# Optimization experiments

Hardware: AMD Instinct MI355X
Metric: run time of the kernel (lower is better)

The kernel has to match this reference:

```python
import jax, jax.numpy as jnp
import numpy as np

NEG_INF = float(-2 ** 31)
B, S, D_IN, D_H, H = 4, 2048, 512, 512, 8


def setup_inputs() -> dict:
    key = jax.random.key(0)
    ks = jax.random.split(key, 11)
    sc_in = 1.0 / np.sqrt(D_IN)
    sc_pr = 1.0 / np.sqrt(D_H * H)
    x = jax.random.normal(ks[0], (B, S, D_IN), dtype=jnp.float32)
    mask = jax.random.randint(ks[1], (B, 1, S), 0, 2, dtype=jnp.int32)
    Wq = jax.random.uniform(ks[2], (H, D_IN, D_H), jnp.float32, -sc_in, sc_in)
    bq = jax.random.uniform(ks[3], (H, D_H), jnp.float32, -sc_in, sc_in)
    Wk = jax.random.uniform(ks[4], (H, D_IN, D_H), jnp.float32, -sc_in, sc_in)
    bk = jax.random.uniform(ks[5], (H, D_H), jnp.float32, -sc_in, sc_in)
    Wv = jax.random.uniform(ks[6], (H, D_IN, D_H), jnp.float32, -sc_in, sc_in)
    bv = jax.random.uniform(ks[7], (H, D_H), jnp.float32, -sc_in, sc_in)
    Wp = jax.random.uniform(ks[8], (H * D_H, D_H), jnp.float32, -sc_pr, sc_pr)
    bp = jax.random.uniform(ks[9], (D_H,), jnp.float32, -sc_pr, sc_pr)
    return {"x": x, "mask": mask, "Wq": Wq, "bq": bq, "Wk": Wk, "bk": bk,
            "Wv": Wv, "bv": bv, "Wp": Wp, "bp": bp}


def reference(x, mask, Wq, bq, Wk, bk, Wv, bv, Wp, bp):
    # per-head Q/K/V projections, batched over the head axis h
    q = jnp.einsum('bsd,hde->bhse', x, Wq) + bq[None, :, None, :]
    k = jnp.einsum('bsd,hde->bhse', x, Wk) + bk[None, :, None, :]
    v = jnp.einsum('bsd,hde->bhse', x, Wv) + bv[None, :, None, :]
    scores = jnp.einsum('bhse,bhte->bhst', q, k) / jnp.sqrt(jnp.float32(D_H))
    scores = jnp.where(mask[:, None, :, :] == 0, NEG_INF, scores)
    probs = jax.nn.softmax(scores, axis=-1)
    out = jnp.einsum('bhst,bhte->bhse', probs, v)  # [B,H,S,D_H]
    cat = out.transpose(0, 2, 1, 3).reshape(B, S, H * D_H)
    return cat @ Wp + bp
```

## Files before the change

### kernel.cpp

```cpp
#include <hip/hip_runtime.h>
#include <hip/hip_bf16.h>
#include <cstdint>
#include <cstddef>

typedef unsigned short ushort_t;
typedef __bf16 bf16x8 __attribute__((ext_vector_type(8)));
typedef float floatx4 __attribute__((ext_vector_type(4)));

#define S_LEN 2048
#define DIN   512
#define DH    512
#define NHEAD 8
#define NBAT  4
#define NBH   32
#define HP    4096

#define MiB (1024ull * 1024ull)
#define WQT_OFF   (0ull)
#define WKT_OFF   (4ull  * MiB)
#define WVT_OFF   (8ull  * MiB)
#define WPT_OFF   (12ull * MiB)
#define XBF_OFF   (16ull * MiB)
#define Q_OFF     (24ull * MiB)
#define K_OFF     (88ull * MiB)
#define VT_OFF    (152ull * MiB)
#define O_OFF     (216ull * MiB)
#define LSUM_OFF  (280ull * MiB)
#define P_OFF     (281ull * MiB)
#define WS_BYTES  (409ull * MiB)

__device__ __align__(256) unsigned char g_ws[WS_BYTES];

__device__ __forceinline__ ushort_t f2bf(float f) {
  union { float f; uint32_t u; } v; v.f = f;
  uint32_t r = v.u + 0x7fffu + ((v.u >> 16) & 1u);
  return (ushort_t)(r >> 16);
}

typedef __attribute__((address_space(3))) uint32_t lds_uint;
typedef __attribute__((address_space(1))) const uint32_t glb_uint;

__device__ __forceinline__ void async16(void* lds, const void* g) {
  __builtin_amdgcn_global_load_lds((glb_uint*)g, (lds_uint*)lds, 16, 0, 0);
}

#define BBAR() do { \
    __builtin_amdgcn_sched_barrier(0); \
    __builtin_amdgcn_s_barrier(); \
    __builtin_amdgcn_sched_barrier(0); \
  } while (0)

#define SG_R(n) __builtin_amdgcn_sched_group_barrier(0x100, (n), 0)
#define SG_M(n) __builtin_amdgcn_sched_group_barrier(0x8,   (n), 0)
#define SG_V(n) __builtin_amdgcn_sched_group_barrier(0x10,  (n), 0)


#define STG_A(dbuf, hh, kt) do { \
    const ushort_t* _g = gA + (size_t)(kt) * 64 + (size_t)(hh) * a128; \
    char* _s = sAh + (dbuf) * 32768 + (hh) * 16384; \
    async16(_s, _g); \
    async16(_s + 8192, _g + a64); \
  } while (0)

#define STG_B(dbuf, hh, kt) do { \
    const ushort_t* _g = gB + (size_t)(kt) * 64 + (size_t)(hh) * b128; \
    char* _s = sBh + (dbuf) * 32768 + (hh) * 16384; \
    async16(_s, _g); \
    async16(_s + 8192, _g + b64); \
  } while (0)

#define LDAF(fi) do { \
    const char* _b = (const char*)As + cur * 32768 + ((fi) >> 2) * 16384 \
                     + (((fi) & 3) << 11) + aoff0; \
    af[fi][0] = *(const bf16x8*)(_b + swz0); \
    af[fi][1] = *(const bf16x8*)(_b + swz1); \
  } while (0)

#define LDBF(fj) do { \
    const char* _b = (const char*)Bs + cur * 32768 + ((fj) >> 1) * 16384 \
                     + (((fj) & 1) << 11) + boff0; \
    bfr[fj][0] = *(const bf16x8*)(_b + swz0); \
    bfr[fj][1] = *(const bf16x8*)(_b + swz1); \
  } while (0)

#define MF2(q, ii, jj, ai, bj) do { \
    acc[q][ii][jj] = __builtin_amdgcn_mfma_f32_16x16x32_bf16(af[ai][0], bfr[bj][0], acc[q][ii][jj], 0, 0, 0); \
    acc[q][ii][jj] = __builtin_amdgcn_mfma_f32_16x16x32_bf16(af[ai][1], bfr[bj][1], acc[q][ii][jj], 0, 0, 0); \
  } while (0)

__device__ __forceinline__ void gemm256_core(
    const ushort_t* __restrict__ A, const ushort_t* __restrict__ Bt,
    int lda, int ldb, int kdim,
    ushort_t* As, ushort_t* Bs, floatx4 acc[4][4][2])
{
  const int t = threadIdx.x;
  const int w = t >> 6, l = t & 63;
  const int l15 = l & 15, lq = l >> 4;
  const int wq_r = w >> 2, wq_c = w & 3;

  const int r0 = t >> 3, c0 = t & 7;
  const ushort_t* gA = A + (size_t)r0 * lda + ((c0 ^ (r0 & 7)) << 3);
  const ushort_t* gB = Bt + (size_t)r0 * ldb + ((c0 ^ (r0 & 7)) << 3);
  const size_t a64 = (size_t)64 * lda, b64 = (size_t)64 * ldb;
  const size_t a128 = (size_t)128 * lda, b128 = (size_t)128 * ldb;
  char* sAh = (char*)As + (w << 10);
  char* sBh = (char*)Bs + (w << 10);

  const int aoff0 = ((wq_r << 6) + l15) << 7;
  const int boff0 = ((wq_c << 5) + l15) << 7;
  const int l7 = l15 & 7;
  const int swz0 = (lq ^ l7) << 4;
  const int swz1 = ((4 + lq) ^ l7) << 4;

  const int nt = kdim >> 6;

#pragma unroll
  for (int q = 0; q < 4; ++q)
#pragma unroll
    for (int i = 0; i < 4; ++i)
#pragma unroll
      for (int j = 0; j < 2; ++j)
        acc[q][i][j] = (floatx4){0.f, 0.f, 0.f, 0.f};

  STG_A(0, 0, 0);
  STG_A(0, 1, 0);
  STG_B(0, 0, 0);
  STG_B(0, 1, 0);
  asm volatile("s_waitcnt vmcnt(0)" ::: "memory");
  BBAR();

  bf16x8 af[8][2], bfr[4][2];

#pragma unroll 1
  for (int tt = 0; tt < nt; ++tt) {
    const int cur = tt & 1, nxt = cur ^ 1;
    const bool more = (tt + 1 < nt);
    LDBF(0); LDBF(1); LDAF(0);
    SG_R(6);
    if (more) STG_A(nxt, 0, tt + 1);
    SG_V(2);
    LDAF(1); SG_R(2); MF2(0,0,0, 0,0); MF2(0,0,1, 0,1); SG_M(4);
    LDAF(2); SG_R(2); MF2(0,1,0, 1,0); MF2(0,1,1, 1,1); SG_M(4);
    LDAF(3); SG_R(2); MF2(0,2,0, 2,0); MF2(0,2,1, 2,1); SG_M(4);
    if (more) STG_A(nxt, 1, tt + 1);
    SG_V(2);
    LDBF(2); SG_R(2); MF2(0,3,0, 3,0); MF2(0,3,1, 3,1); SG_M(4);
    LDBF(3); SG_R(2); MF2(1,0,0, 0,2); MF2(1,1,0, 1,2); SG_M(4);
    if (more) STG_B(nxt, 0, tt + 1);
    SG_V(2);
    LDAF(4); SG_R(2); MF2(1,2,0, 2,2); MF2(1,3,0, 3,2); SG_M(4);
    LDAF(5); SG_R(2); MF2(1,0,1, 0,3); MF2(1,1,1, 1,3); SG_M(4);
    LDAF(6); SG_R(2); MF2(1,2,1, 2,3); MF2(1,3,1, 3,3); SG_M(4);
    if (more) STG_B(nxt, 1, tt + 1);
    SG_V(2);
    LDAF(7); SG_R(2); MF2(2,0,0, 4,2); MF2(2,1,0, 5,2); SG_M(4);
    MF2(2,2,0, 6,2); MF2(2,3,0, 7,2); SG_M(4);
    MF2(2,0,1, 4,3); MF2(2,1,1, 5,3); SG_M(4);
    MF2(2,2,1, 6,3); MF2(2,3,1, 7,3); SG_M(4);
    MF2(3,0,0, 4,0); MF2(3,1,0, 5,0); SG_M(4);
    MF2(3,2,0, 6,0); MF2(3,3,0, 7,0); SG_M(4);
    MF2(3,0,1, 4,1); MF2(3,1,1, 5,1); SG_M(4);
    MF2(3,2,1, 6,1); MF2(3,3,1, 7,1); SG_M(4);
    asm volatile("s_waitcnt vmcnt(0)" ::: "memory");
    __builtin_amdgcn_s_barrier();
  }
}

__device__ __forceinline__ void gemm_core(
    const ushort_t* __restrict__ A, const ushort_t* __restrict__ Bt,
    int lda, int ldb, int kdim,
    ushort_t* As, ushort_t* Bs, floatx4 acc[4][4])
{
  const int t = threadIdx.x;
  const int w = t >> 6;
  const int l = t & 63;
  const int wrow = w >> 1, wcol = w & 1;
  const int l15 = l & 15, lq = l >> 4;

  const ushort_t* gA = A + (size_t)(t >> 2) * lda + (t & 3) * 8;
  const ushort_t* gB = Bt + (size_t)(t >> 2) * ldb + (t & 3) * 8;
  const size_t strideA = (size_t)64 * lda;
  const size_t strideB = (size_t)64 * ldb;
  char* ldsA0 = (char*)As + w * 1024;
  char* ldsB0 = (char*)Bs + w * 1024;

  async16(ldsA0,        gA);
  async16(ldsA0 + 4096, gA + strideA);
  async16(ldsB0,        gB);
  async16(ldsB0 + 4096, gB + strideB);

#pragma unroll
  for (int i = 0; i < 4; ++i)
#pragma unroll
    for (int j = 0; j < 4; ++j)
      acc[i][j] = (floatx4){0.f, 0.f, 0.f, 0.f};

  const int nwin = kdim >> 5;
#pragma unroll 1
  for (int k = 0; k < nwin; ++k) {
    __syncthreads();
    const int cur = k & 1;
    if (k + 1 < nwin) {
      const int nxt = cur ^ 1;
      const ushort_t* gA1 = gA + (size_t)(k + 1) * 32;
      const ushort_t* gB1 = gB + (size_t)(k + 1) * 32;
      char* ldsA1 = ldsA0 + nxt * 8192;
      char* ldsB1 = ldsB0 + nxt * 8192;
      async16(ldsA1,        gA1);
      async16(ldsA1 + 4096, gA1 + strideA);
      async16(ldsB1,        gB1);
      async16(ldsB1 + 4096, gB1 + strideB);
    }
    const ushort_t* rdA = As + cur * 4096 + (wrow * 64 + l15) * 32 + lq * 8;
    const ushort_t* rdB = Bs + cur * 4096 + (wcol * 64 + l15) * 32 + lq * 8;

    bf16x8 aft[4], bfrt[4];
#pragma unroll
    for (int i = 0; i < 4; ++i) aft[i] = *(const bf16x8*)(rdA + i * 512);
#pragma unroll
    for (int j = 0; j < 4; ++j) bfrt[j] = *(const bf16x8*)(rdB + j * 512);
#pragma unroll
    for (int i = 0; i < 4; ++i)
#pragma unroll
      for (int j = 0; j < 4; ++j)
        acc[i][j] = __builtin_amdgcn_mfma_f32_16x16x32_bf16(aft[i], bfrt[j], acc[i][j], 0, 0, 0);
  }
}

__global__ __launch_bounds__(256) void convert_f32_bf16(
    const float* __restrict__ src, size_t dstOff, int n)
{
  ushort_t* dst = (ushort_t*)(g_ws + dstOff);
  int i = (blockIdx.x * 256 + threadIdx.x) * 4;
  if (i >= n) return;
  float4 v = *(const float4*)(src + i);
  ushort_t o[4] = {f2bf(v.x), f2bf(v.y), f2bf(v.z), f2bf(v.w)};
  *(uint2*)(dst + i) = *(const uint2*)o;
}

__global__ __launch_bounds__(256) void transpose_f32_bf16(
    const float* __restrict__ src, size_t dstOff, int R, int C)
{
  __shared__ ushort_t tile[32][33];
  ushort_t* dst = (ushort_t*)(g_ws + dstOff) + (size_t)blockIdx.z * R * C;
  src += (size_t)blockIdx.z * R * C;
  int r0 = blockIdx.y * 32, c0 = blockIdx.x * 32;
  int tx = threadIdx.x & 31, ty = threadIdx.x >> 5;
  for (int i = ty; i < 32; i += 8)
    tile[i][tx] = f2bf(src[(size_t)(r0 + i) * C + (c0 + tx)]);
  __syncthreads();
  for (int i = ty; i < 32; i += 8)
    dst[(size_t)(c0 + i) * R + (r0 + tx)] = tile[tx][i];
}

__global__ __launch_bounds__(256) void zero_lsum()
{
  float* lsum = (float*)(g_ws + LSUM_OFF);
  int i = (blockIdx.x * 256 + threadIdx.x) * 4;
  *(float4*)(lsum + i) = (float4){0.f, 0.f, 0.f, 0.f};
}

__global__ __launch_bounds__(512, 2) void qkv_gemm(
    const float* __restrict__ bq, const float* __restrict__ bk,
    const float* __restrict__ bv)
{
  __shared__ __align__(16) ushort_t SH[65536];
  ushort_t* As = SH;
  ushort_t* Bs = SH + 32768;
  const int z = blockIdx.z;
  const int bh = z & 31, sel = z >> 5, b = bh >> 3, h = bh & 7;
  const size_t wOff = (sel == 0) ? WQT_OFF : (sel == 1) ? WKT_OFF : WVT_OFF;
  const float* bias = ((sel == 0) ? bq : (sel == 1) ? bk : bv) + h * DH;
  const int tileM = blockIdx.y * 256, tileN = blockIdx.x * 256;

  const ushort_t* A  = (const ushort_t*)(g_ws + XBF_OFF)
                       + ((size_t)b * S_LEN + tileM) * DIN;
  const ushort_t* Bt = (const ushort_t*)(g_ws + wOff)
                       + ((size_t)h * DH + tileN) * DIN;
  floatx4 acc[4][4][2];
  gemm256_core(A, Bt, DIN, DIN, DIN, As, Bs, acc);

  const int t = threadIdx.x, w = t >> 6, l = t & 63;
  const int l15 = l & 15, lq = l >> 4;
  const int wq_r = w >> 2, wq_c = w & 3;
  const int QM[4] = {0, 0, 1, 1}, QN[4] = {0, 1, 1, 0};

  if (sel == 2) {
    char* SB = (char*)SH;
    BBAR();
#pragma unroll
    for (int q = 0; q < 4; ++q) {
#pragma unroll
      for (int j = 0; j < 2; ++j) {
        const int nl = QN[q] * 128 + wq_c * 32 + j * 16 + l15;
        const float bsn = bias[tileN + nl];
#pragma unroll
        for (int i = 0; i < 4; ++i) {
          const int ml = QM[q] * 128 + wq_r * 64 + i * 16 + lq * 4;
          ushort_t pk[4];
#pragma unroll
          for (int r = 0; r < 4; ++r) pk[r] = f2bf(acc[q][i][j][r] + bsn);
          const int byte = nl * 512 + (((ml >> 3) ^ (nl & 7)) << 4) + (ml & 7) * 2;
          *(uint2*)(SB + byte) = *(const uint2*)pk;
        }
      }
    }
    BBAR();
    ushort_t* VTb = (ushort_t*)(g_ws + VT_OFF)
                    + ((size_t)bh * DH + tileN) * S_LEN + tileM;
#pragma unroll
    for (int s = 0; s < 16; ++s) {
      const int nl = (w << 5) + (s << 1) + (l >> 5);
      const int c  = l & 31;
      const uint4 v = *(const uint4*)(SB + nl * 512 + ((c ^ (nl & 7)) << 4));
      *(uint4*)(VTb + (size_t)nl * S_LEN + c * 8) = v;
    }
  } else {
    ushort_t* Db = (ushort_t*)(g_ws + ((sel == 0) ? Q_OFF : K_OFF));
#pragma unroll
    for (int q = 0; q < 4; ++q) {
#pragma unroll
      for (int j = 0; j < 2; ++j) {
        const int n = tileN + QN[q] * 128 + wq_c * 32 + j * 16 + l15;
        const float bsn = bias[n];
#pragma unroll
        for (int i = 0; i < 4; ++i) {
#pragma unroll
          for (int r = 0; r < 4; ++r) {
            const int m = tileM + QM[q] * 128 + wq_r * 64 + i * 16 + lq * 4 + r;
            Db[((size_t)bh * S_LEN + m) * DH + n] = f2bf(acc[q][i][j][r] + bsn);
          }
        }
      }
    }
  }
}

__global__ __launch_bounds__(512, 2) void scores_kernel(
    const int* __restrict__ mask, int c0)
{
  __shared__ __align__(16) ushort_t SH[65536];
  ushort_t* As = SH;
  ushort_t* Bs = SH + 32768;
  const int hl = blockIdx.z, bh = c0 + hl, b = bh >> 3;
  const int tileM = blockIdx.y * 256, tileN = blockIdx.x * 256;

  const ushort_t* A  = (const ushort_t*)(g_ws + Q_OFF)
                       + ((size_t)bh * S_LEN + tileM) * DH;
  const ushort_t* Bt = (const ushort_t*)(g_ws + K_OFF)
                       + ((size_t)bh * S_LEN + tileN) * DH;
  floatx4 acc[4][4][2];
  gemm256_core(A, Bt, DH, DH, DH, As, Bs, acc);

  const float scale = 0.04419417382415922f;
  const int t = threadIdx.x, w = t >> 6, l = t & 63;
  const int l15 = l & 15, lq = l >> 4;
  const int wq_r = w >> 2, wq_c = w & 3;
  const int QM[4] = {0, 0, 1, 1}, QN[4] = {0, 1, 1, 0};
  ushort_t* Pp = (ushort_t*)(g_ws + P_OFF) + (size_t)hl * S_LEN * S_LEN;
  const int* mask_b = mask + (size_t)b * S_LEN;
  float* lsum = (float*)(g_ws + LSUM_OFF);

  float rsum[2][4][4];
#pragma unroll
  for (int qm = 0; qm < 2; ++qm)
#pragma unroll
    for (int i = 0; i < 4; ++i)
#pragma unroll
      for (int r = 0; r < 4; ++r) rsum[qm][i][r] = 0.f;

#pragma unroll
  for (int q = 0; q < 4; ++q) {
#pragma unroll
    for (int j = 0; j < 2; ++j) {
      const int n = tileN + QN[q] * 128 + wq_c * 32 + j * 16 + l15;
      const int mv = mask_b[n];
#pragma unroll
      for (int i = 0; i < 4; ++i) {
#pragma unroll
        for (int r = 0; r < 4; ++r) {
          const int m = tileM + QM[q] * 128 + wq_r * 64 + i * 16 + lq * 4 + r;
          float s = fminf(acc[q][i][j][r] * scale, 30.f);
          const float p = mv ? __expf(s) : 0.f;
          rsum[QM[q]][i][r] += p;
          Pp[(size_t)m * S_LEN + n] = f2bf(p);
        }
      }
    }
  }
#pragma unroll
  for (int qm = 0; qm < 2; ++qm) {
#pragma unroll
    for (int i = 0; i < 4; ++i) {
#pragma unroll
      for (int r = 0; r < 4; ++r) {
        float v = rsum[qm][i][r];
        v += __shfl_xor(v, 1);
        v += __shfl_xor(v, 2);
        v += __shfl_xor(v, 4);
        v += __shfl_xor(v, 8);
        if (l15 == 0) {
          const int m = tileM + qm * 128 + wq_r * 64 + i * 16 + lq * 4 + r;
          atomicAdd(&lsum[(size_t)hl * S_LEN + m], v);
        }
      }
    }
  }
}

__global__ __launch_bounds__(512, 2) void pv_kernel(int c0)
{
  __shared__ __align__(16) ushort_t SH[65536];
  ushort_t* As = SH;
  ushort_t* Bs = SH + 32768;
  const int hl = blockIdx.z, bh = c0 + hl, b = bh >> 3, h = bh & 7;
  const int tileM = blockIdx.y * 256, tileN = blockIdx.x * 256;

  const ushort_t* A  = (const ushort_t*)(g_ws + P_OFF)
                       + (size_t)hl * S_LEN * S_LEN + (size_t)tileM * S_LEN;
  const ushort_t* Bt = (const ushort_t*)(g_ws + VT_OFF)
                       + ((size_t)bh * DH + tileN) * S_LEN;
  floatx4 acc[4][4][2];
  gemm256_core(A, Bt, S_LEN, S_LEN, S_LEN, As, Bs, acc);

  const float* lsum = (const float*)(g_ws + LSUM_OFF);
  ushort_t* Ob = (ushort_t*)(g_ws + O_OFF);
  const int t = threadIdx.x, w = t >> 6, l = t & 63;
  const int l15 = l & 15, lq = l >> 4;
  const int wq_r = w >> 2, wq_c = w & 3;
  const int QM[4] = {0, 0, 1, 1}, QN[4] = {0, 1, 1, 0};
#pragma unroll
  for (int q = 0; q < 4; ++q) {
#pragma unroll
    for (int i = 0; i < 4; ++i) {
#pragma unroll
      for (int r = 0; r < 4; ++r) {
        const int m = tileM + QM[q] * 128 + wq_r * 64 + i * 16 + lq * 4 + r;
        const float lv = lsum[(size_t)hl * S_LEN + m];
        const float inv = (lv > 1e-20f) ? 1.0f / lv : 0.f;
#pragma unroll
        for (int j = 0; j < 2; ++j) {
          const int n = tileN + QN[q] * 128 + wq_c * 32 + j * 16 + l15;
          Ob[((size_t)b * S_LEN + m) * HP + h * DH + n] =
              f2bf(acc[q][i][j][r] * inv);
        }
      }
    }
  }
}

__global__ __launch_bounds__(256) void proj_kernel(
    const float* __restrict__ bp, float* __restrict__ out)
{
  __shared__ __align__(16) ushort_t As[2 * 128 * 32], Bs[2 * 128 * 32];
  const int tileM = blockIdx.y * 128, tileN = blockIdx.x * 128;

  const ushort_t* A  = (const ushort_t*)(g_ws + O_OFF) + (size_t)tileM * HP;
  const ushort_t* Bt = (const ushort_t*)(g_ws + WPT_OFF) + (size_t)tileN * HP;
  floatx4 acc[4][4];
  gemm_core(A, Bt, HP, HP, HP, As, Bs, acc);

  const int t = threadIdx.x, w = t >> 6, l = t & 63;
  const int wrow = w >> 1, wcol = w & 1, l15 = l & 15, lq = l >> 4;
#pragma unroll
  for (int j = 0; j < 4; ++j) {
    const int n = tileN + wcol * 64 + j * 16 + l15;
    const float bsn = bp[n];
#pragma unroll
    for (int i = 0; i < 4; ++i) {
#pragma unroll
      for (int r = 0; r < 4; ++r) {
        const int m = tileM + wrow * 64 + i * 16 + lq * 4 + r;
        out[(size_t)m * DH + n] = acc[i][j][r] + bsn;
      }
    }
  }
}

extern "C" void kernel_launch(void* const* d_in, const int* in_sizes, int n_in,
                              void* d_out, int out_size, void* d_ws, size_t ws_size,
                              hipStream_t stream) {
  const float* x  = (const float*)d_in[0];
  const int*   msk= (const int*)d_in[1];
  const float* Wq = (const float*)d_in[2];
  const float* bq = (const float*)d_in[3];
  const float* Wk = (const float*)d_in[4];
  const float* bk = (const float*)d_in[5];
  const float* Wv = (const float*)d_in[6];
  const float* bv = (const float*)d_in[7];
  const float* Wp = (const float*)d_in[8];
  const float* bp = (const float*)d_in[9];
  float* out = (float*)d_out;

  convert_f32_bf16<<<dim3(NBAT * S_LEN * DIN / 1024), 256, 0, stream>>>(
      x, XBF_OFF, NBAT * S_LEN * DIN);

  transpose_f32_bf16<<<dim3(16, 16, NHEAD), 256, 0, stream>>>(Wq, WQT_OFF, DIN, DH);
  transpose_f32_bf16<<<dim3(16, 16, NHEAD), 256, 0, stream>>>(Wk, WKT_OFF, DIN, DH);
  transpose_f32_bf16<<<dim3(16, 16, NHEAD), 256, 0, stream>>>(Wv, WVT_OFF, DIN, DH);
  transpose_f32_bf16<<<dim3(16, 128, 1),    256, 0, stream>>>(Wp, WPT_OFF, HP, DH);

  qkv_gemm<<<dim3(2, 8, 3 * NBH), 512, 0, stream>>>(bq, bk, bv);

  for (int c0 = 0; c0 < NBH; c0 += 16) {
    zero_lsum<<<dim3(32), 256, 0, stream>>>();
    scores_kernel<<<dim3(8, 8, 16), 512, 0, stream>>>(msk, c0);
    pv_kernel<<<dim3(2, 8, 16), 512, 0, stream>>>(c0);
  }

  proj_kernel<<<dim3(DH / 128, (NBAT * S_LEN) / 128), 256, 0, stream>>>(bp, out);
}
```

Measured before the change: 744.4 us.

## Split-K the projection GEMM with 256-tiles and reorder score blocks by head

```diff
diff --git a/kernel.cpp b/kernel.cpp
--- a/kernel.cpp
+++ b/kernel.cpp
@@ -166,67 +166,6 @@
   }
 }
 
-__device__ __forceinline__ void gemm_core(
-    const ushort_t* __restrict__ A, const ushort_t* __restrict__ Bt,
-    int lda, int ldb, int kdim,
-    ushort_t* As, ushort_t* Bs, floatx4 acc[4][4])
-{
-  const int t = threadIdx.x;
-  const int w = t >> 6;
-  const int l = t & 63;
-  const int wrow = w >> 1, wcol = w & 1;
-  const int l15 = l & 15, lq = l >> 4;
-
-  const ushort_t* gA = A + (size_t)(t >> 2) * lda + (t & 3) * 8;
-  const ushort_t* gB = Bt + (size_t)(t >> 2) * ldb + (t & 3) * 8;
-  const size_t strideA = (size_t)64 * lda;
-  const size_t strideB = (size_t)64 * ldb;
-  char* ldsA0 = (char*)As + w * 1024;
-  char* ldsB0 = (char*)Bs + w * 1024;
-
-  async16(ldsA0,        gA);
-  async16(ldsA0 + 4096, gA + strideA);
-  async16(ldsB0,        gB);
-  async16(ldsB0 + 4096, gB + strideB);
-
-#pragma unroll
-  for (int i = 0; i < 4; ++i)
-#pragma unroll
-    for (int j = 0; j < 4; ++j)
-      acc[i][j] = (floatx4){0.f, 0.f, 0.f, 0.f};
-
-  const int nwin = kdim >> 5;
-#pragma unroll 1
-  for (int k = 0; k < nwin; ++k) {
-    __syncthreads();
-    const int cur = k & 1;
-    if (k + 1 < nwin) {
-      const int nxt = cur ^ 1;
-      const ushort_t* gA1 = gA + (size_t)(k + 1) * 32;
-      const ushort_t* gB1 = gB + (size_t)(k + 1) * 32;
-      char* ldsA1 = ldsA0 + nxt * 8192;
-      char* ldsB1 = ldsB0 + nxt * 8192;
-      async16(ldsA1,        gA1);
-      async16(ldsA1 + 4096, gA1 + strideA);
-      async16(ldsB1,        gB1);
-      async16(ldsB1 + 4096, gB1 + strideB);
-    }
-    const ushort_t* rdA = As + cur * 4096 + (wrow * 64 + l15) * 32 + lq * 8;
-    const ushort_t* rdB = Bs + cur * 4096 + (wcol * 64 + l15) * 32 + lq * 8;
-
-    bf16x8 aft[4], bfrt[4];
-#pragma unroll
-    for (int i = 0; i < 4; ++i) aft[i] = *(const bf16x8*)(rdA + i * 512);
-#pragma unroll
-    for (int j = 0; j < 4; ++j) bfrt[j] = *(const bf16x8*)(rdB + j * 512);
-#pragma unroll
-    for (int i = 0; i < 4; ++i)
-#pragma unroll
-      for (int j = 0; j < 4; ++j)
-        acc[i][j] = __builtin_amdgcn_mfma_f32_16x16x32_bf16(aft[i], bfrt[j], acc[i][j], 0, 0, 0);
-  }
-}
-
 __global__ __launch_bounds__(256) void convert_f32_bf16(
     const float* __restrict__ src, size_t dstOff, int n)
 {
@@ -260,6 +199,12 @@
   *(float4*)(lsum + i) = (float4){0.f, 0.f, 0.f, 0.f};
 }
 
+__global__ __launch_bounds__(256) void zero_out(float* __restrict__ out)
+{
+  int i = (blockIdx.x * 256 + threadIdx.x) * 4;
+  *(float4*)(out + i) = (float4){0.f, 0.f, 0.f, 0.f};
+}
+
 __global__ __launch_bounds__(512, 2) void qkv_gemm(
     const float* __restrict__ bq, const float* __restrict__ bk,
     const float* __restrict__ bv)
@@ -337,13 +282,16 @@
 }
 
 __global__ __launch_bounds__(512, 2) void scores_kernel(
-    const int* __restrict__ mask, int c0)
+    const int* __restrict__ mask, int cbase)
 {
   __shared__ __align__(16) ushort_t SH[65536];
   ushort_t* As = SH;
   ushort_t* Bs = SH + 32768;
-  const int hl = blockIdx.z, bh = c0 + hl, b = bh >> 3;
-  const int tileM = blockIdx.y * 256, tileN = blockIdx.x * 256;
+  const int bid = blockIdx.x;
+  const int hl8 = bid & 7, tl = bid >> 3;
+  const int tileM = (tl & 7) * 256, tileN = (tl >> 3) * 256;
+  const int bh = cbase + hl8, b = bh >> 3;
+  const int hl16 = bh & 15;
 
   const ushort_t* A  = (const ushort_t*)(g_ws + Q_OFF)
                        + ((size_t)bh * S_LEN + tileM) * DH;
@@ -357,7 +305,7 @@
   const int l15 = l & 15, lq = l >> 4;
   const int wq_r = w >> 2, wq_c = w & 3;
   const int QM[4] = {0, 0, 1, 1}, QN[4] = {0, 1, 1, 0};
-  ushort_t* Pp = (ushort_t*)(g_ws + P_OFF) + (size_t)hl * S_LEN * S_LEN;
+  ushort_t* Pp = (ushort_t*)(g_ws + P_OFF) + (size_t)hl16 * S_LEN * S_LEN;
   const int* mask_b = mask + (size_t)b * S_LEN;
   float* lsum = (float*)(g_ws + LSUM_OFF);
 
@@ -401,7 +349,7 @@
         v += __shfl_xor(v, 8);
         if (l15 == 0) {
           const int m = tileM + qm * 128 + wq_r * 64 + i * 16 + lq * 4 + r;
-          atomicAdd(&lsum[(size_t)hl * S_LEN + m], v);
+          atomicAdd(&lsum[(size_t)hl16 * S_LEN + m], v);
         }
       }
     }
@@ -449,29 +397,39 @@
   }
 }
 
-__global__ __launch_bounds__(256) void proj_kernel(
+__global__ __launch_bounds__(512, 2) void proj_kernel(
     const float* __restrict__ bp, float* __restrict__ out)
 {
-  __shared__ __align__(16) ushort_t As[2 * 128 * 32], Bs[2 * 128 * 32];
-  const int tileM = blockIdx.y * 128, tileN = blockIdx.x * 128;
-
-  const ushort_t* A  = (const ushort_t*)(g_ws + O_OFF) + (size_t)tileM * HP;
-  const ushort_t* Bt = (const ushort_t*)(g_ws + WPT_OFF) + (size_t)tileN * HP;
-  floatx4 acc[4][4];
-  gemm_core(A, Bt, HP, HP, HP, As, Bs, acc);
+  __shared__ __align__(16) ushort_t SH[65536];
+  ushort_t* As = SH;
+  ushort_t* Bs = SH + 32768;
+  const int tileM = blockIdx.y * 256, tileN = blockIdx.x * 256;
+  const int ks = blockIdx.z;
+
+  const ushort_t* A  = (const ushort_t*)(g_ws + O_OFF)
+                       + (size_t)tileM * HP + ks * 1024;
+  const ushort_t* Bt = (const ushort_t*)(g_ws + WPT_OFF)
+                       + (size_t)tileN * HP + ks * 1024;
+  floatx4 acc[4][4][2];
+  gemm256_core(A, Bt, HP, HP, 1024, As, Bs, acc);
 
   const int t = threadIdx.x, w = t >> 6, l = t & 63;
-  const int wrow = w >> 1, wcol = w & 1, l15 = l & 15, lq = l >> 4;
-#pragma unroll
-  for (int j = 0; j < 4; ++j) {
-    const int n = tileN + wcol * 64 + j * 16 + l15;
-    const float bsn = bp[n];
-#pragma unroll
-    for (int i = 0; i < 4; ++i) {
-#pragma unroll
-      for (int r = 0; r < 4; ++r) {
-        const int m = tileM + wrow * 64 + i * 16 + lq * 4 + r;
-        out[(size_t)m * DH + n] = acc[i][j][r] + bsn;
+  const int l15 = l & 15, lq = l >> 4;
+  const int wq_r = w >> 2, wq_c = w & 3;
+  const int QM[4] = {0, 0, 1, 1}, QN[4] = {0, 1, 1, 0};
+#pragma unroll
+  for (int q = 0; q < 4; ++q) {
+#pragma unroll
+    for (int j = 0; j < 2; ++j) {
+      const int n = tileN + QN[q] * 128 + wq_c * 32 + j * 16 + l15;
+      const float bsn = (ks == 0) ? bp[n] : 0.f;
+#pragma unroll
+      for (int i = 0; i < 4; ++i) {
+#pragma unroll
+        for (int r = 0; r < 4; ++r) {
+          const int m = tileM + QM[q] * 128 + wq_r * 64 + i * 16 + lq * 4 + r;
+          atomicAdd(&out[(size_t)m * DH + n], acc[q][i][j][r] + bsn);
+        }
       }
     }
   }
@@ -499,14 +457,16 @@
   transpose_f32_bf16<<<dim3(16, 16, NHEAD), 256, 0, stream>>>(Wk, WKT_OFF, DIN, DH);
   transpose_f32_bf16<<<dim3(16, 16, NHEAD), 256, 0, stream>>>(Wv, WVT_OFF, DIN, DH);
   transpose_f32_bf16<<<dim3(16, 128, 1),    256, 0, stream>>>(Wp, WPT_OFF, HP, DH);
+  zero_out<<<dim3(NBAT * S_LEN * DH / 1024), 256, 0, stream>>>(out);
 
   qkv_gemm<<<dim3(2, 8, 3 * NBH), 512, 0, stream>>>(bq, bk, bv);
 
-  for (int c0 = 0; c0 < NBH; c0 += 16) {
+  for (int c16 = 0; c16 < NBH; c16 += 16) {
     zero_lsum<<<dim3(32), 256, 0, stream>>>();
-    scores_kernel<<<dim3(8, 8, 16), 512, 0, stream>>>(msk, c0);
-    pv_kernel<<<dim3(2, 8, 16), 512, 0, stream>>>(c0);
-  }
-
-  proj_kernel<<<dim3(DH / 128, (NBAT * S_LEN) / 128), 256, 0, stream>>>(bp, out);
-}
+    scores_kernel<<<dim3(512), 512, 0, stream>>>(msk, c16);
+    scores_kernel<<<dim3(512), 512, 0, stream>>>(msk, c16 + 8);
+    pv_kernel<<<dim3(2, 8, 16), 512, 0, stream>>>(c16);
+  }
+
+  proj_kernel<<<dim3(2, 32, 4), 512, 0, stream>>>(bp, out);
+}
```

Measured after the change: 723.8 us. 2.8% less time.
